# Optimization experiments

Measured on AMD Instinct MI355X. Metric: run time of the kernel, lower is better.

## Reference

```python
import jax, jax.numpy as jnp
import numpy as np

# DCRNN (PEMS-BAY scale) constants
N = 325      # num_nodes
B = 64       # batch_size
T = 12       # encoder seq_len
HZ = 12      # decoder horizon
U = 64       # rnn_units
DIN = 2      # input_dim
DOUT = 1     # output_dim
K = 2        # max_diffusion_step
NM = K + 1   # num diffusion matrices (Chebyshev, single laplacian support)


def _glorot(key, shape):
    lim = float(np.sqrt(6.0 / (shape[0] + shape[1])))
    return jax.random.uniform(key, shape, jnp.float32, -lim, lim)


def setup_inputs() -> dict:
    key = jax.random.key(0)
    ks = jax.random.split(key, 8)
    # random symmetric adjacency -> scaled Laplacian support (lambda_max ~= 2 approx)
    a = np.asarray(jax.random.uniform(ks[0], (N, N)))
    a = (a + a.T) * 0.5
    a = a * (a > 0.9)
    d = a.sum(1)
    dinv = 1.0 / np.sqrt(np.maximum(d, 1e-8))
    L = np.eye(N, dtype=np.float32) - (dinv[:, None] * a * dinv[None, :]).astype(np.float32)
    support = jnp.asarray(L - np.eye(N, dtype=np.float32))  # 2L/lambda_max - I with lambda_max=2

    def cell_params(k, din):
        f = (din + U) * NM
        k1, k2 = jax.random.split(k)
        return dict(gate_W=_glorot(k1, (f, 2 * U)), gate_b=jnp.zeros((2 * U,), jnp.float32),
                    cand_W=_glorot(k2, (f, U)), cand_b=jnp.zeros((U,), jnp.float32))

    inp = {"inputs": jax.random.normal(ks[1], (T, B, N * DIN), jnp.float32),
           "support": support}
    for name, din, kk in [("enc0", DIN, ks[2]), ("enc1", U, ks[3]),
                          ("dec0", DOUT, ks[4]), ("dec1", U, ks[5])]:
        for pn, v in cell_params(kk, din).items():
            inp[f"{name}_{pn}"] = v
    inp["proj_W"] = _glorot(ks[6], (U, DOUT))
    inp["proj_b"] = jnp.zeros((DOUT,), jnp.float32)
    return inp


def _gconv(x, support, W, b):
    # x: (B, N, F). Chebyshev diffusion: x0=x, x1=Lx, x2=2Lx1-x0, ...
    xs = [x]
    x0, x1 = x, jnp.einsum('mn,bnf->bmf', support, x)
    xs.append(x1)
    for _ in range(2, K + 1):
        x2 = 2.0 * jnp.einsum('mn,bnf->bmf', support, x1) - x0
        xs.append(x2)
        x0, x1 = x1, x2
    xk = jnp.concatenate(xs, axis=-1)  # (B, N, NM*F)
    return xk @ W + b


def _gru_cell(x, h, support, gW, gb, cW, cb):
    # diffusion-conv GRU: r,u gates then candidate
    ru = jax.nn.sigmoid(_gconv(jnp.concatenate([x, h], -1), support, gW, gb))
    r, u = jnp.split(ru, 2, axis=-1)
    c = jnp.tanh(_gconv(jnp.concatenate([x, r * h], -1), support, cW, cb))
    return u * h + (1.0 - u) * c


def reference(inputs, support,
              enc0_gate_W, enc0_gate_b, enc0_cand_W, enc0_cand_b,
              enc1_gate_W, enc1_gate_b, enc1_cand_W, enc1_cand_b,
              dec0_gate_W, dec0_gate_b, dec0_cand_W, dec0_cand_b,
              dec1_gate_W, dec1_gate_b, dec1_cand_W, dec1_cand_b,
              proj_W, proj_b):
    x_seq = inputs.reshape(T, B, N, DIN)
    h0 = jnp.zeros((B, N, U), inputs.dtype)

    def enc_step(carry, x):
        h_l0, h_l1 = carry
        h_l0 = _gru_cell(x, h_l0, support, enc0_gate_W, enc0_gate_b, enc0_cand_W, enc0_cand_b)
        h_l1 = _gru_cell(h_l0, h_l1, support, enc1_gate_W, enc1_gate_b, enc1_cand_W, enc1_cand_b)
        return (h_l0, h_l1), None

    (h_l0, h_l1), _ = jax.lax.scan(enc_step, (h0, h0), x_seq)

    def dec_step(carry, _):
        d_in, hd0, hd1 = carry
        hd0 = _gru_cell(d_in, hd0, support, dec0_gate_W, dec0_gate_b, dec0_cand_W, dec0_cand_b)
        hd1 = _gru_cell(hd0, hd1, support, dec1_gate_W, dec1_gate_b, dec1_cand_W, dec1_cand_b)
        out = hd1 @ proj_W + proj_b  # (B, N, DOUT)
        return (out, hd0, hd1), out.reshape(B, N * DOUT)

    start = jnp.zeros((B, N, DOUT), inputs.dtype)  # GO symbol
    _, outputs = jax.lax.scan(dec_step, (start, h_l0, h_l1), None, length=HZ)
    return outputs  # (horizon, B, N*DOUT)
```

## Files before the change

### kernel.cpp

```cpp
#include <hip/hip_runtime.h>

constexpr int N  = 325;
constexpr int B  = 64;
constexpr int T  = 12;
constexpr int HZ = 12;
constexpr int U  = 64;
constexpr int BN = B * N;

constexpr int SSTIL = 42;
constexpr int SSKC  = 11;
constexpr int XST   = 364;

typedef __attribute__((ext_vector_type(8))) short short8;
typedef __attribute__((ext_vector_type(4))) float floatx4;

__device__ inline unsigned short f2bf(float f) {
    unsigned u = __float_as_uint(f);
    u += 0x7fff + ((u >> 16) & 1);
    return (unsigned short)(u >> 16);
}
__device__ inline unsigned pack_hilo(float v) {
    const unsigned short hi = f2bf(v);
    const float hif = __uint_as_float(((unsigned)hi) << 16);
    const unsigned short lo = f2bf(v - hif);
    return (unsigned)hi | ((unsigned)lo << 16);
}
__device__ inline void unpack8(const uint4 u0, const uint4 u1,
                               short8& h, short8& l) {
    const unsigned uu[8] = {u0.x, u0.y, u0.z, u0.w, u1.x, u1.y, u1.z, u1.w};
    #pragma unroll
    for (int j = 0; j < 8; ++j) {
        h[j] = (short)(uu[j] & 0xffffu);
        l[j] = (short)(uu[j] >> 16);
    }
}


__global__ void zero_kernel(unsigned* __restrict__ p, long n) {
    long i = (long)blockIdx.x * blockDim.x + threadIdx.x;
    const long stride = (long)gridDim.x * blockDim.x;
    for (; i < n; i += stride) p[i] = 0u;
}

__global__ __launch_bounds__(256)
void s2_build(const float* __restrict__ S, float* __restrict__ S2)
{
    const int m = blockIdx.x;
    __shared__ float srow[N];
    for (int i = threadIdx.x; i < N; i += 256) srow[i] = S[m * N + i];
    __syncthreads();
    for (int c = threadIdx.x; c < N; c += 256) {
        float a = 0.f;
        for (int k = 0; k < N; ++k) a += srow[k] * S[k * N + c];
        S2[m * N + c] = a;
    }
}

__global__ __launch_bounds__(64)
void prepack_ss(const float* __restrict__ S, const float* __restrict__ S2,
                short* __restrict__ ssh, short* __restrict__ ssl)
{
    const int t = blockIdx.x, kc = blockIdx.y, lane = threadIdx.x;
    const int quad = lane >> 4, l15 = lane & 15;
    short8 hv, lv;
    #pragma unroll
    for (int j = 0; j < 8; ++j) {
        const int m = t * 16 + l15;
        const int k = kc * 32 + quad * 8 + j;
        float v = 0.f;
        if (k < N) {
            if (m < N) v = S[m * N + k];
            else if (m >= 336 && m < 336 + N) v = S2[(m - 336) * N + k];
        }
        const unsigned short hb = f2bf(v);
        hv[j] = (short)hb;
        lv[j] = (short)f2bf(v - __uint_as_float(((unsigned)hb) << 16));
    }
    const size_t off = ((size_t)(t * SSKC + kc) * 64 + lane);
    ((short8*)ssh)[off] = hv;
    ((short8*)ssl)[off] = lv;
}

__global__ __launch_bounds__(64)
void prepack_w(const float* __restrict__ W, short* __restrict__ Wh,
               short* __restrict__ Wl, int F, int Nout, int NT)
{
    const int kc = blockIdx.x, n = blockIdx.y, lane = threadIdx.x;
    const int quad = lane >> 4, l15 = lane & 15;
    short8 hv, lv;
    #pragma unroll
    for (int j = 0; j < 8; ++j) {
        const int k   = kc * 32 + quad * 8 + j;
        const int col = n * 16 + l15;
        const int lvl = k / F, f = k - lvl * F;
        float w = 0.f;
        if (lvl == 0)
            w = W[(size_t)f * Nout + col] - W[(size_t)(2 * F + f) * Nout + col];
        else if (lvl == 1)
            w = W[(size_t)(F + f) * Nout + col];
        else if (lvl == 2)
            w = 2.f * W[(size_t)(2 * F + f) * Nout + col];
        const unsigned short hb = f2bf(w);
        hv[j] = (short)hb;
        lv[j] = (short)f2bf(w - __uint_as_float(((unsigned)hb) << 16));
    }
    const size_t off = ((size_t)(kc * NT + n) * 64 + lane);
    ((short8*)Wh)[off] = hv;
    ((short8*)Wl)[off] = lv;
}

template<int DIN, int F, int K3P, bool RMUL, bool VEC>
__device__ __forceinline__ void diffuse_body(
    const short8* __restrict__ ssh, const short8* __restrict__ ssl,
    const float* __restrict__ x, const float* __restrict__ h,
    const float* __restrict__ ru, unsigned* __restrict__ zcat,
    int cx, int b, unsigned* __restrict__ xls)
{
    const int c0 = cx * 32;
    const int tid = threadIdx.x, wave = tid >> 6, lane = tid & 63;
    const int quad = lane >> 4, l15 = lane & 15;

    if constexpr (VEC) {
        for (int idx4 = tid; idx4 < 352 * 8; idx4 += 896) {
            const int n = idx4 >> 3, f = (idx4 & 7) * 4, gf = c0 + f;
            uint4 pk = make_uint4(0u, 0u, 0u, 0u);
            if (n < N) {
                const int row = b * N + n;
                float4 v;
                if (gf < DIN) {
                    v = *(const float4*)&x[(size_t)row * DIN + gf];
                } else {
                    v = *(const float4*)&h[(size_t)row * U + (gf - DIN)];
                    if (RMUL) {
                        const float4 rv = *(const float4*)&ru[(size_t)row * 128 + (gf - DIN)];
                        v.x *= rv.x; v.y *= rv.y; v.z *= rv.z; v.w *= rv.w;
                    }
                }
                pk.x = pack_hilo(v.x); pk.y = pack_hilo(v.y);
                pk.z = pack_hilo(v.z); pk.w = pack_hilo(v.w);
                if (!(RMUL && gf < DIN))
                    *(uint4*)&zcat[(size_t)row * K3P + gf] = pk;
            }
            xls[(f + 0) * XST + n] = pk.x;
            xls[(f + 1) * XST + n] = pk.y;
            xls[(f + 2) * XST + n] = pk.z;
            xls[(f + 3) * XST + n] = pk.w;
        }
    } else {
        for (int idx = tid; idx < 352 * 32; idx += 896) {
            const int n = idx >> 5, f = idx & 31, gf = c0 + f;
            unsigned u = 0u;
            if (n < N && gf < F) {
                const int row = b * N + n;
                float v;
                if (gf < DIN) {
                    v = x[(size_t)row * DIN + gf];
                } else {
                    v = h[(size_t)row * U + (gf - DIN)];
                    if (RMUL) v *= ru[(size_t)row * 128 + (gf - DIN)];
                }
                u = pack_hilo(v);
                if (!(RMUL && gf < DIN))
                    zcat[(size_t)row * K3P + gf] = u;
            }
            xls[f * XST + n] = u;
        }
    }
    __syncthreads();

    const int tb = wave * 3;

    floatx4 acc[3][2];
    #pragma unroll
    for (int i = 0; i < 3; ++i)
        #pragma unroll
        for (int n = 0; n < 2; ++n)
            acc[i][n] = (floatx4){0.f, 0.f, 0.f, 0.f};

    short8 cah[3], cal[3], nah[3], nal[3];
    #pragma unroll
    for (int i = 0; i < 3; ++i) {
        const size_t fo = (size_t)((tb + i) * SSKC) * 64 + lane;
        cah[i] = ssh[fo]; cal[i] = ssl[fo];
    }
    for (int kc = 0; kc < SSKC; ++kc) {
        if (kc + 1 < SSKC) {
            #pragma unroll
            for (int i = 0; i < 3; ++i) {
                const size_t fo = (size_t)((tb + i) * SSKC + kc + 1) * 64 + lane;
                nah[i] = ssh[fo]; nal[i] = ssl[fo];
            }
        }
        short8 bh[2], bl[2];
        const int koff = kc * 32 + quad * 8;
        #pragma unroll
        for (int n = 0; n < 2; ++n) {
            const uint4 u0 = *(const uint4*)&xls[(n * 16 + l15) * XST + koff];
            const uint4 u1 = *(const uint4*)&xls[(n * 16 + l15) * XST + koff + 4];
            unpack8(u0, u1, bh[n], bl[n]);
        }
        #pragma unroll
        for (int i = 0; i < 3; ++i)
            #pragma unroll
            for (int n = 0; n < 2; ++n) {
                acc[i][n] = __builtin_amdgcn_mfma_f32_16x16x32_bf16(cah[i], bh[n], acc[i][n], 0, 0, 0);
                acc[i][n] = __builtin_amdgcn_mfma_f32_16x16x32_bf16(cah[i], bl[n], acc[i][n], 0, 0, 0);
                acc[i][n] = __builtin_amdgcn_mfma_f32_16x16x32_bf16(cal[i], bh[n], acc[i][n], 0, 0, 0);
            }
        if (kc + 1 < SSKC) {
            #pragma unroll
            for (int i = 0; i < 3; ++i) { cah[i] = nah[i]; cal[i] = nal[i]; }
        }
    }

    #pragma unroll
    for (int i = 0; i < 3; ++i) {
        const int t = tb + i;
        #pragma unroll
        for (int n = 0; n < 2; ++n) {
            const int col = c0 + n * 16 + l15;
            if (col >= F) continue;
            #pragma unroll
            for (int r = 0; r < 4; ++r) {
                const int m = t * 16 + quad * 4 + r;
                if (m < N)
                    zcat[(size_t)(b * N + m) * K3P + F + col] = pack_hilo(acc[i][n][r]);
                else if (m >= 336 && m < 336 + N)
                    zcat[(size_t)(b * N + (m - 336)) * K3P + 2 * F + col] = pack_hilo(acc[i][n][r]);
            }
        }
    }
}


__device__ __forceinline__ void gate_body(const unsigned* __restrict__ zcat,
    int K3p, const short8* __restrict__ Wh, const short8* __restrict__ Wl,
    const float* __restrict__ bias, float* __restrict__ ru, int bx, int nb)
{
    constexpr int NT = 4;
    const int tid = threadIdx.x, wave = tid >> 6, lane = tid & 63;
    const int quad = lane >> 4, l15 = lane & 15;
    const int row0 = bx * 64 + wave * 16;

    floatx4 acc[NT];
    #pragma unroll
    for (int n = 0; n < NT; ++n) {
        const float bv = bias[(nb + n) * 16 + l15];
        acc[n] = (floatx4){bv, bv, bv, bv};
    }
    const unsigned* __restrict__ zrow = zcat + (size_t)(row0 + l15) * K3p + quad * 8;
    const int KC = K3p >> 5;
    for (int kc = 0; kc < KC; ++kc) {
        const uint4* p = (const uint4*)(zrow + kc * 32);
        short8 ahi, alo;
        unpack8(p[0], p[1], ahi, alo);
        const short8* __restrict__ wh = Wh + (size_t)(kc * 8 + nb) * 64 + lane;
        const short8* __restrict__ wl = Wl + (size_t)(kc * 8 + nb) * 64 + lane;
        #pragma unroll
        for (int n = 0; n < NT; ++n) {
            const short8 bh = wh[n * 64], bl = wl[n * 64];
            acc[n] = __builtin_amdgcn_mfma_f32_16x16x32_bf16(ahi, bh, acc[n], 0, 0, 0);
            acc[n] = __builtin_amdgcn_mfma_f32_16x16x32_bf16(ahi, bl, acc[n], 0, 0, 0);
            acc[n] = __builtin_amdgcn_mfma_f32_16x16x32_bf16(alo, bh, acc[n], 0, 0, 0);
        }
    }
    #pragma unroll
    for (int n = 0; n < NT; ++n) {
        const int col = (nb + n) * 16 + l15;
        #pragma unroll
        for (int r = 0; r < 4; ++r) {
            const int row = row0 + quad * 4 + r;
            ru[(size_t)row * 128 + col] = 1.f / (1.f + __expf(-acc[n][r]));
        }
    }
}

__device__ __forceinline__ void cand_body(const unsigned* __restrict__ zcat,
    int K3p, const short8* __restrict__ Wh, const short8* __restrict__ Wl,
    const float* __restrict__ bias, const float* __restrict__ ru,
    float* __restrict__ h, int bx, int nb)
{
    constexpr int NT = 2;
    const int tid = threadIdx.x, wave = tid >> 6, lane = tid & 63;
    const int quad = lane >> 4, l15 = lane & 15;
    const int row0 = bx * 64 + wave * 16;

    floatx4 acc[NT];
    #pragma unroll
    for (int n = 0; n < NT; ++n) {
        const float bv = bias[(nb + n) * 16 + l15];
        acc[n] = (floatx4){bv, bv, bv, bv};
    }
    const unsigned* __restrict__ zrow = zcat + (size_t)(row0 + l15) * K3p + quad * 8;
    const int KC = K3p >> 5;
    for (int kc = 0; kc < KC; ++kc) {
        const uint4* p = (const uint4*)(zrow + kc * 32);
        short8 ahi, alo;
        unpack8(p[0], p[1], ahi, alo);
        const short8* __restrict__ wh = Wh + (size_t)(kc * 4 + nb) * 64 + lane;
        const short8* __restrict__ wl = Wl + (size_t)(kc * 4 + nb) * 64 + lane;
        #pragma unroll
        for (int n = 0; n < NT; ++n) {
            const short8 bh = wh[n * 64], bl = wl[n * 64];
            acc[n] = __builtin_amdgcn_mfma_f32_16x16x32_bf16(ahi, bh, acc[n], 0, 0, 0);
            acc[n] = __builtin_amdgcn_mfma_f32_16x16x32_bf16(ahi, bl, acc[n], 0, 0, 0);
            acc[n] = __builtin_amdgcn_mfma_f32_16x16x32_bf16(alo, bh, acc[n], 0, 0, 0);
        }
    }
    #pragma unroll
    for (int n = 0; n < NT; ++n) {
        const int col = (nb + n) * 16 + l15;
        #pragma unroll
        for (int r = 0; r < 4; ++r) {
            const int row = row0 + quad * 4 + r;
            const float c  = tanhf(acc[n][r]);
            const float ug = ru[(size_t)row * 128 + 64 + col];
            const float hv = h[(size_t)row * 64 + col];
            h[(size_t)row * 64 + col] = ug * hv + (1.f - ug) * c;
        }
    }
}


template<int DIN, int F, int K3P, bool RMUL, int CB, bool VEC>
__global__ __launch_bounds__(896, 7)
void diffuse_solo(const short8* __restrict__ ssh, const short8* __restrict__ ssl,
                  const float* __restrict__ x, const float* __restrict__ h,
                  const float* __restrict__ ru, unsigned* __restrict__ zcat)
{
    __shared__ __align__(16) unsigned xls[32 * XST];
    diffuse_body<DIN, F, K3P, RMUL, VEC>(ssh, ssl, x, h, ru, zcat,
                                         CB + blockIdx.x, blockIdx.y, xls);
}

__global__ __launch_bounds__(256)
void gate_solo(const unsigned* __restrict__ zcat, int K3p,
               const short8* __restrict__ Wh, const short8* __restrict__ Wl,
               const float* __restrict__ bias, float* __restrict__ ru)
{
    gate_body(zcat, K3p, Wh, Wl, bias, ru, blockIdx.x, blockIdx.y * 4);
}

__global__ __launch_bounds__(256)
void cand_solo(const unsigned* __restrict__ zcat, int K3p,
               const short8* __restrict__ Wh, const short8* __restrict__ Wl,
               const float* __restrict__ bias, const float* __restrict__ ru,
               float* __restrict__ h)
{
    cand_body(zcat, K3p, Wh, Wl, bias, ru, h, blockIdx.x, blockIdx.y * 2);
}

__global__ __launch_bounds__(256)
void cand_proj(const unsigned* __restrict__ zcat, int K3p,
               const short8* __restrict__ Wh, const short8* __restrict__ Wl,
               const float* __restrict__ bias, const float* __restrict__ ru,
               float* __restrict__ h, const float* __restrict__ pW,
               const float* __restrict__ pb, float* __restrict__ outp,
               float* __restrict__ dec_in)
{
    constexpr int NT = 4;
    const int tid = threadIdx.x, wave = tid >> 6, lane = tid & 63;
    const int quad = lane >> 4, l15 = lane & 15;
    const int row0 = blockIdx.x * 64 + wave * 16;

    floatx4 acc[NT];
    #pragma unroll
    for (int n = 0; n < NT; ++n) {
        const float bv = bias[n * 16 + l15];
        acc[n] = (floatx4){bv, bv, bv, bv};
    }
    const unsigned* __restrict__ zrow = zcat + (size_t)(row0 + l15) * K3p + quad * 8;
    const int KC = K3p >> 5;
    for (int kc = 0; kc < KC; ++kc) {
        const uint4* p = (const uint4*)(zrow + kc * 32);
        short8 ahi, alo;
        unpack8(p[0], p[1], ahi, alo);
        const short8* __restrict__ wh = Wh + (size_t)(kc * 4) * 64 + lane;
        const short8* __restrict__ wl = Wl + (size_t)(kc * 4) * 64 + lane;
        #pragma unroll
        for (int n = 0; n < NT; ++n) {
            const short8 bh = wh[n * 64], bl = wl[n * 64];
            acc[n] = __builtin_amdgcn_mfma_f32_16x16x32_bf16(ahi, bh, acc[n], 0, 0, 0);
            acc[n] = __builtin_amdgcn_mfma_f32_16x16x32_bf16(ahi, bl, acc[n], 0, 0, 0);
            acc[n] = __builtin_amdgcn_mfma_f32_16x16x32_bf16(alo, bh, acc[n], 0, 0, 0);
        }
    }
    float pr[4] = {0.f, 0.f, 0.f, 0.f};
    #pragma unroll
    for (int n = 0; n < NT; ++n) {
        const int col = n * 16 + l15;
        const float pw = pW[col];
        #pragma unroll
        for (int r = 0; r < 4; ++r) {
            const int row = row0 + quad * 4 + r;
            const float c  = tanhf(acc[n][r]);
            const float ug = ru[(size_t)row * 128 + 64 + col];
            const float hv = h[(size_t)row * 64 + col];
            const float hn = ug * hv + (1.f - ug) * c;
            h[(size_t)row * 64 + col] = hn;
            pr[r] += hn * pw;
        }
    }
    #pragma unroll
    for (int r = 0; r < 4; ++r) {
        float v = pr[r];
        v += __shfl_xor(v, 1); v += __shfl_xor(v, 2);
        v += __shfl_xor(v, 4); v += __shfl_xor(v, 8);
        if (l15 == 0) {
            const int row = row0 + quad * 4 + r;
            const float o = v + pb[0];
            outp[row]   = o;
            dec_in[row] = o;
        }
    }
}


struct DuoDP {
    const short8 *ssh, *ssl;
    const float *xA, *hA, *ruA; unsigned* zA;
    const float *xB, *hB, *ruB; unsigned* zB;
    int cA;
    int cbB;
};

template<bool RM>
__global__ __launch_bounds__(896, 7)
void diffuse_duo(DuoDP P)
{
    __shared__ __align__(16) unsigned xls[32 * XST];
    if ((int)blockIdx.x < P.cA)
        diffuse_body<2, 66, 224, RM, false>(P.ssh, P.ssl, P.xA, P.hA, P.ruA,
                                            P.zA, blockIdx.x, blockIdx.y, xls);
    else
        diffuse_body<64, 128, 384, RM, true>(P.ssh, P.ssl, P.xB, P.hB, P.ruB,
                                             P.zB, P.cbB + blockIdx.x - P.cA,
                                             blockIdx.y, xls);
}

struct DuoGP {
    const unsigned* zA; const short8 *WhA, *WlA; const float* bA; float* ruA;
    const unsigned* zB; const short8 *WhB, *WlB; const float* bB; float* ruB;
};

__global__ __launch_bounds__(256)
void gate_duo(DuoGP P)
{
    if (blockIdx.z == 0)
        gate_body(P.zA, 224, P.WhA, P.WlA, P.bA, P.ruA, blockIdx.x, blockIdx.y * 4);
    else
        gate_body(P.zB, 384, P.WhB, P.WlB, P.bB, P.ruB, blockIdx.x, blockIdx.y * 4);
}

struct DuoCP {
    const unsigned* zA; const short8 *WhA, *WlA; const float* bA;
    const float* ruA; float* hA;
    const unsigned* zB; const short8 *WhB, *WlB; const float* bB;
    const float* ruB; float* hB;
};

__global__ __launch_bounds__(256)
void cand_duo(DuoCP P)
{
    if (blockIdx.z == 0)
        cand_body(P.zA, 224, P.WhA, P.WlA, P.bA, P.ruA, P.hA, blockIdx.x, blockIdx.y * 2);
    else
        cand_body(P.zB, 384, P.WhB, P.WlB, P.bB, P.ruB, P.hB, blockIdx.x, blockIdx.y * 2);
}


extern "C" void kernel_launch(void* const* d_in, const int* in_sizes, int n_in,
                              void* d_out, int out_size, void* d_ws, size_t ws_size,
                              hipStream_t stream)
{
    const float* inputs = (const float*)d_in[0];
    const float* S      = (const float*)d_in[1];
    const float* Wt[4][4];
    for (int l = 0; l < 4; ++l)
        for (int j = 0; j < 4; ++j)
            Wt[l][j] = (const float*)d_in[2 + l * 4 + j];
    const float* pW = (const float*)d_in[18];
    const float* pb = (const float*)d_in[19];
    float* out = (float*)d_out;

    float*    ws     = (float*)d_ws;
    float*    h0     = ws;
    float*    h1     = h0 + (size_t)BN * U;
    float*    dec_in = h1 + (size_t)BN * U;
    float*    ruA    = dec_in + BN;
    float*    ruB    = ruA + (size_t)BN * 128;
    unsigned* zcatA  = (unsigned*)(ruB + (size_t)BN * 128);
    unsigned* zcatB  = zcatA + (size_t)BN * 224;
    float*    S2     = (float*)(zcatB + (size_t)BN * 384);
    char*     pp     = (char*)(S2 + (size_t)N * N);
    pp = (char*)(((uintptr_t)pp + 15) & ~(uintptr_t)15);

    short* ssh = (short*)pp;
    short* ssl = ssh + (size_t)SSTIL * SSKC * 64 * 8;
    char*  wpbase = (char*)(ssl + (size_t)SSTIL * SSKC * 64 * 8);

    const int Fs[4]   = {66, 128, 65, 128};
    const int K3ps[4] = {224, 384, 224, 384};
    short *Wgh[4], *Wgl[4], *Wch[4], *Wcl[4];
    size_t off = 0;
    for (int l = 0; l < 4; ++l) {
        const size_t ge = (size_t)K3ps[l] * 128, ce = (size_t)K3ps[l] * 64;
        Wgh[l] = (short*)(wpbase + off); off += ge * 2;
        Wgl[l] = (short*)(wpbase + off); off += ge * 2;
        Wch[l] = (short*)(wpbase + off); off += ce * 2;
        Wcl[l] = (short*)(wpbase + off); off += ce * 2;
    }

    const long zn = (long)BN * (2 * U) + BN + (long)BN * 256 + (long)BN * (224 + 384);
    zero_kernel<<<2048, 256, 0, stream>>>((unsigned*)h0, zn);

    s2_build<<<N, 256, 0, stream>>>(S, S2);
    prepack_ss<<<dim3(SSTIL, SSKC), 64, 0, stream>>>(S, S2, ssh, ssl);
    for (int l = 0; l < 4; ++l) {
        prepack_w<<<dim3(K3ps[l] / 32, 8), 64, 0, stream>>>(Wt[l][0], Wgh[l], Wgl[l],
                                                            Fs[l], 128, 8);
        prepack_w<<<dim3(K3ps[l] / 32, 4), 64, 0, stream>>>(Wt[l][2], Wch[l], Wcl[l],
                                                            Fs[l], 64, 4);
    }

    const short8* SSH = (const short8*)ssh;
    const short8* SSL = (const short8*)ssl;

    for (int s = 0; s <= T; ++s) {
        const float* x0 = inputs + (size_t)s * BN * 2;
        const bool a = (s < T), b1 = (s >= 1);
        if (a && b1) {
            DuoDP dp{SSH, SSL, x0, h0, nullptr, zcatA, h0, h1, nullptr, zcatB, 3, 0};
            diffuse_duo<false><<<dim3(7, B), 896, 0, stream>>>(dp);
            DuoGP gp{zcatA, (short8*)Wgh[0], (short8*)Wgl[0], Wt[0][1], ruA,
                     zcatB, (short8*)Wgh[1], (short8*)Wgl[1], Wt[1][1], ruB};
            gate_duo<<<dim3(BN / 64, 2, 2), 256, 0, stream>>>(gp);
            DuoDP dp2{SSH, SSL, x0, h0, ruA, zcatA, h0, h1, ruB, zcatB, 3, 2};
            diffuse_duo<true><<<dim3(5, B), 896, 0, stream>>>(dp2);
            DuoCP cp{zcatA, (short8*)Wch[0], (short8*)Wcl[0], Wt[0][3], ruA, h0,
                     zcatB, (short8*)Wch[1], (short8*)Wcl[1], Wt[1][3], ruB, h1};
            cand_duo<<<dim3(BN / 64, 2, 2), 256, 0, stream>>>(cp);
        } else if (a) {
            diffuse_solo<2, 66, 224, false, 0, false><<<dim3(3, B), 896, 0, stream>>>(
                SSH, SSL, x0, h0, nullptr, zcatA);
            gate_solo<<<dim3(BN / 64, 2), 256, 0, stream>>>(
                zcatA, 224, (short8*)Wgh[0], (short8*)Wgl[0], Wt[0][1], ruA);
            diffuse_solo<2, 66, 224, true, 0, false><<<dim3(3, B), 896, 0, stream>>>(
                SSH, SSL, x0, h0, ruA, zcatA);
            cand_solo<<<dim3(BN / 64, 2), 256, 0, stream>>>(
                zcatA, 224, (short8*)Wch[0], (short8*)Wcl[0], Wt[0][3], ruA, h0);
        } else {
            diffuse_solo<64, 128, 384, false, 0, true><<<dim3(4, B), 896, 0, stream>>>(
                SSH, SSL, h0, h1, nullptr, zcatB);
            gate_solo<<<dim3(BN / 64, 2), 256, 0, stream>>>(
                zcatB, 384, (short8*)Wgh[1], (short8*)Wgl[1], Wt[1][1], ruB);
            diffuse_solo<64, 128, 384, true, 2, true><<<dim3(2, B), 896, 0, stream>>>(
                SSH, SSL, h0, h1, ruB, zcatB);
            cand_solo<<<dim3(BN / 64, 2), 256, 0, stream>>>(
                zcatB, 384, (short8*)Wch[1], (short8*)Wcl[1], Wt[1][3], ruB, h1);
        }
    }

    for (int hz = 0; hz < HZ; ++hz) {
        diffuse_solo<1, 65, 224, false, 0, false><<<dim3(3, B), 896, 0, stream>>>(
            SSH, SSL, dec_in, h0, nullptr, zcatB);
        gate_solo<<<dim3(BN / 64, 2), 256, 0, stream>>>(
            zcatB, 224, (short8*)Wgh[2], (short8*)Wgl[2], Wt[2][1], ruA);
        diffuse_solo<1, 65, 224, true, 0, false><<<dim3(3, B), 896, 0, stream>>>(
            SSH, SSL, dec_in, h0, ruA, zcatB);
        cand_solo<<<dim3(BN / 64, 2), 256, 0, stream>>>(
            zcatB, 224, (short8*)Wch[2], (short8*)Wcl[2], Wt[2][3], ruA, h0);
        diffuse_solo<64, 128, 384, false, 0, true><<<dim3(4, B), 896, 0, stream>>>(
            SSH, SSL, h0, h1, nullptr, zcatB);
        gate_solo<<<dim3(BN / 64, 2), 256, 0, stream>>>(
            zcatB, 384, (short8*)Wgh[3], (short8*)Wgl[3], Wt[3][1], ruA);
        diffuse_solo<64, 128, 384, true, 2, true><<<dim3(2, B), 896, 0, stream>>>(
            SSH, SSL, h0, h1, ruA, zcatB);
        cand_proj<<<BN / 64, 256, 0, stream>>>(
            zcatB, 384, (short8*)Wch[3], (short8*)Wcl[3], Wt[3][3], ruA, h1,
            pW, pb, out + (size_t)hz * BN, dec_in);
    }
}
```

Before: 4.080 ms.

## Read level-0 diffusion input directly in gate/cand GEMMs instead of staging in zcat

The diffusion kernels no longer write the packed hi/lo copy of the raw input [x, h] (or [x, r*h]) into zcat. The gate and candidate GEMMs now rebuild those first K-chunks on the fly from the fp32 x, h and r buffers, and only the diffused levels are read from zcat. Prepacked weights are reordered to match, with the level-0 block padded to whole 32-wide chunks. Because the candidate step now reads h while writing a new h, the hidden states are double-buffered (ping-pong). This removes a global write and read of roughly a third of zcat per step, at the cost of extra pack_hilo work and some padding MFMAs inside the GEMMs.

New measurement: 3.964 ms (median of 2 runs). 1.03x faster.

```diff
diff --git a/kernel.cpp b/kernel.cpp
--- a/kernel.cpp
+++ b/kernel.cpp
@@ -83,23 +83,27 @@
 
 __global__ __launch_bounds__(64)
 void prepack_w(const float* __restrict__ W, short* __restrict__ Wh,
-               short* __restrict__ Wl, int F, int Nout, int NT)
+               short* __restrict__ Wl, int F, int Nout, int NT, int Z0KC)
 {
     const int kc = blockIdx.x, n = blockIdx.y, lane = threadIdx.x;
     const int quad = lane >> 4, l15 = lane & 15;
     short8 hv, lv;
     #pragma unroll
     for (int j = 0; j < 8; ++j) {
-        const int k   = kc * 32 + quad * 8 + j;
+        const int p   = kc * 32 + quad * 8 + j;
         const int col = n * 16 + l15;
-        const int lvl = k / F, f = k - lvl * F;
         float w = 0.f;
-        if (lvl == 0)
-            w = W[(size_t)f * Nout + col] - W[(size_t)(2 * F + f) * Nout + col];
-        else if (lvl == 1)
-            w = W[(size_t)(F + f) * Nout + col];
-        else if (lvl == 2)
-            w = 2.f * W[(size_t)(2 * F + f) * Nout + col];
+        if (p < Z0KC * 32) {
+            const int f = p;
+            if (f < F)
+                w = W[(size_t)f * Nout + col] - W[(size_t)(2 * F + f) * Nout + col];
+        } else {
+            const int q = p - Z0KC * 32;
+            if (q < F)
+                w = W[(size_t)(F + q) * Nout + col];
+            else if (q < 2 * F)
+                w = 2.f * W[(size_t)(2 * F + (q - F)) * Nout + col];
+        }
         const unsigned short hb = f2bf(w);
         hv[j] = (short)hb;
         lv[j] = (short)f2bf(w - __uint_as_float(((unsigned)hb) << 16));
@@ -109,7 +113,54 @@
     ((short8*)Wl)[off] = lv;
 }
 
-template<int DIN, int F, int K3P, bool RMUL, bool VEC>
+template<int DIN, int F, bool RM, bool ZV>
+__device__ __forceinline__ void z0_frag(const float* __restrict__ x,
+    const float* __restrict__ h, const float* __restrict__ ru,
+    int row, int kc, int quad, short8& ah, short8& al)
+{
+    float v[8];
+    if constexpr (ZV) {
+        const int k0 = kc * 32 + quad * 8;
+        if (k0 < 64) {
+            const float4 a = *(const float4*)&x[(size_t)row * 64 + k0];
+            const float4 b = *(const float4*)&x[(size_t)row * 64 + k0 + 4];
+            v[0]=a.x; v[1]=a.y; v[2]=a.z; v[3]=a.w;
+            v[4]=b.x; v[5]=b.y; v[6]=b.z; v[7]=b.w;
+        } else {
+            const int kk = k0 - 64;
+            float4 a = *(const float4*)&h[(size_t)row * 64 + kk];
+            float4 b = *(const float4*)&h[(size_t)row * 64 + kk + 4];
+            if constexpr (RM) {
+                const float4 ra = *(const float4*)&ru[(size_t)row * 128 + kk];
+                const float4 rb = *(const float4*)&ru[(size_t)row * 128 + kk + 4];
+                a.x *= ra.x; a.y *= ra.y; a.z *= ra.z; a.w *= ra.w;
+                b.x *= rb.x; b.y *= rb.y; b.z *= rb.z; b.w *= rb.w;
+            }
+            v[0]=a.x; v[1]=a.y; v[2]=a.z; v[3]=a.w;
+            v[4]=b.x; v[5]=b.y; v[6]=b.z; v[7]=b.w;
+        }
+    } else {
+        #pragma unroll
+        for (int j = 0; j < 8; ++j) {
+            const int k = kc * 32 + quad * 8 + j;
+            float t = 0.f;
+            if (k < DIN) t = x[(size_t)row * DIN + k];
+            else if (k < F) {
+                t = h[(size_t)row * 64 + (k - DIN)];
+                if constexpr (RM) t *= ru[(size_t)row * 128 + (k - DIN)];
+            }
+            v[j] = t;
+        }
+    }
+    #pragma unroll
+    for (int j = 0; j < 8; ++j) {
+        const unsigned u = pack_hilo(v[j]);
+        ah[j] = (short)(u & 0xffffu);
+        al[j] = (short)(u >> 16);
+    }
+}
+
+template<int DIN, int F, int YP, bool RMUL, bool VEC>
 __device__ __forceinline__ void diffuse_body(
     const short8* __restrict__ ssh, const short8* __restrict__ ssl,
     const float* __restrict__ x, const float* __restrict__ h,
@@ -138,8 +189,6 @@
                 }
                 pk.x = pack_hilo(v.x); pk.y = pack_hilo(v.y);
                 pk.z = pack_hilo(v.z); pk.w = pack_hilo(v.w);
-                if (!(RMUL && gf < DIN))
-                    *(uint4*)&zcat[(size_t)row * K3P + gf] = pk;
             }
             xls[(f + 0) * XST + n] = pk.x;
             xls[(f + 1) * XST + n] = pk.y;
@@ -160,8 +209,6 @@
                     if (RMUL) v *= ru[(size_t)row * 128 + (gf - DIN)];
                 }
                 u = pack_hilo(v);
-                if (!(RMUL && gf < DIN))
-                    zcat[(size_t)row * K3P + gf] = u;
             }
             xls[f * XST + n] = u;
         }
@@ -224,23 +271,26 @@
             for (int r = 0; r < 4; ++r) {
                 const int m = t * 16 + quad * 4 + r;
                 if (m < N)
-                    zcat[(size_t)(b * N + m) * K3P + F + col] = pack_hilo(acc[i][n][r]);
+                    zcat[(size_t)(b * N + m) * YP + col] = pack_hilo(acc[i][n][r]);
                 else if (m >= 336 && m < 336 + N)
-                    zcat[(size_t)(b * N + (m - 336)) * K3P + 2 * F + col] = pack_hilo(acc[i][n][r]);
+                    zcat[(size_t)(b * N + (m - 336)) * YP + F + col] = pack_hilo(acc[i][n][r]);
             }
         }
     }
 }
 
 
+template<int DIN, int F, int Z0KC, int YKC, bool ZV>
 __device__ __forceinline__ void gate_body(const unsigned* __restrict__ zcat,
-    int K3p, const short8* __restrict__ Wh, const short8* __restrict__ Wl,
-    const float* __restrict__ bias, float* __restrict__ ru, int bx, int nb)
-{
-    constexpr int NT = 4;
+    const float* __restrict__ x, const float* __restrict__ h,
+    const short8* __restrict__ Wh, const short8* __restrict__ Wl,
+    const float* __restrict__ bias, float* __restrict__ ruout, int bx, int nb)
+{
+    constexpr int YP = YKC * 32, NT = 4;
     const int tid = threadIdx.x, wave = tid >> 6, lane = tid & 63;
     const int quad = lane >> 4, l15 = lane & 15;
     const int row0 = bx * 64 + wave * 16;
+    const int row = row0 + l15;
 
     floatx4 acc[NT];
     #pragma unroll
@@ -248,12 +298,9 @@
         const float bv = bias[(nb + n) * 16 + l15];
         acc[n] = (floatx4){bv, bv, bv, bv};
     }
-    const unsigned* __restrict__ zrow = zcat + (size_t)(row0 + l15) * K3p + quad * 8;
-    const int KC = K3p >> 5;
-    for (int kc = 0; kc < KC; ++kc) {
-        const uint4* p = (const uint4*)(zrow + kc * 32);
+    for (int kc = 0; kc < Z0KC; ++kc) {
         short8 ahi, alo;
-        unpack8(p[0], p[1], ahi, alo);
+        z0_frag<DIN, F, false, ZV>(x, h, nullptr, row, kc, quad, ahi, alo);
         const short8* __restrict__ wh = Wh + (size_t)(kc * 8 + nb) * 64 + lane;
         const short8* __restrict__ wl = Wl + (size_t)(kc * 8 + nb) * 64 + lane;
         #pragma unroll
@@ -264,41 +311,13 @@
             acc[n] = __builtin_amdgcn_mfma_f32_16x16x32_bf16(alo, bh, acc[n], 0, 0, 0);
         }
     }
-    #pragma unroll
-    for (int n = 0; n < NT; ++n) {
-        const int col = (nb + n) * 16 + l15;
-        #pragma unroll
-        for (int r = 0; r < 4; ++r) {
-            const int row = row0 + quad * 4 + r;
-            ru[(size_t)row * 128 + col] = 1.f / (1.f + __expf(-acc[n][r]));
-        }
-    }
-}
-
-__device__ __forceinline__ void cand_body(const unsigned* __restrict__ zcat,
-    int K3p, const short8* __restrict__ Wh, const short8* __restrict__ Wl,
-    const float* __restrict__ bias, const float* __restrict__ ru,
-    float* __restrict__ h, int bx, int nb)
-{
-    constexpr int NT = 2;
-    const int tid = threadIdx.x, wave = tid >> 6, lane = tid & 63;
-    const int quad = lane >> 4, l15 = lane & 15;
-    const int row0 = bx * 64 + wave * 16;
-
-    floatx4 acc[NT];
-    #pragma unroll
-    for (int n = 0; n < NT; ++n) {
-        const float bv = bias[(nb + n) * 16 + l15];
-        acc[n] = (floatx4){bv, bv, bv, bv};
-    }
-    const unsigned* __restrict__ zrow = zcat + (size_t)(row0 + l15) * K3p + quad * 8;
-    const int KC = K3p >> 5;
-    for (int kc = 0; kc < KC; ++kc) {
+    const unsigned* __restrict__ zrow = zcat + (size_t)row * YP + quad * 8;
+    for (int kc = 0; kc < YKC; ++kc) {
         const uint4* p = (const uint4*)(zrow + kc * 32);
         short8 ahi, alo;
         unpack8(p[0], p[1], ahi, alo);
-        const short8* __restrict__ wh = Wh + (size_t)(kc * 4 + nb) * 64 + lane;
-        const short8* __restrict__ wl = Wl + (size_t)(kc * 4 + nb) * 64 + lane;
+        const short8* __restrict__ wh = Wh + (size_t)((Z0KC + kc) * 8 + nb) * 64 + lane;
+        const short8* __restrict__ wl = Wl + (size_t)((Z0KC + kc) * 8 + nb) * 64 + lane;
         #pragma unroll
         for (int n = 0; n < NT; ++n) {
             const short8 bh = wh[n * 64], bl = wl[n * 64];
@@ -312,71 +331,36 @@
         const int col = (nb + n) * 16 + l15;
         #pragma unroll
         for (int r = 0; r < 4; ++r) {
-            const int row = row0 + quad * 4 + r;
-            const float c  = tanhf(acc[n][r]);
-            const float ug = ru[(size_t)row * 128 + 64 + col];
-            const float hv = h[(size_t)row * 64 + col];
-            h[(size_t)row * 64 + col] = ug * hv + (1.f - ug) * c;
-        }
-    }
-}
-
-
-template<int DIN, int F, int K3P, bool RMUL, int CB, bool VEC>
-__global__ __launch_bounds__(896, 7)
-void diffuse_solo(const short8* __restrict__ ssh, const short8* __restrict__ ssl,
-                  const float* __restrict__ x, const float* __restrict__ h,
-                  const float* __restrict__ ru, unsigned* __restrict__ zcat)
-{
-    __shared__ __align__(16) unsigned xls[32 * XST];
-    diffuse_body<DIN, F, K3P, RMUL, VEC>(ssh, ssl, x, h, ru, zcat,
-                                         CB + blockIdx.x, blockIdx.y, xls);
-}
-
-__global__ __launch_bounds__(256)
-void gate_solo(const unsigned* __restrict__ zcat, int K3p,
-               const short8* __restrict__ Wh, const short8* __restrict__ Wl,
-               const float* __restrict__ bias, float* __restrict__ ru)
-{
-    gate_body(zcat, K3p, Wh, Wl, bias, ru, blockIdx.x, blockIdx.y * 4);
-}
-
-__global__ __launch_bounds__(256)
-void cand_solo(const unsigned* __restrict__ zcat, int K3p,
-               const short8* __restrict__ Wh, const short8* __restrict__ Wl,
-               const float* __restrict__ bias, const float* __restrict__ ru,
-               float* __restrict__ h)
-{
-    cand_body(zcat, K3p, Wh, Wl, bias, ru, h, blockIdx.x, blockIdx.y * 2);
-}
-
-__global__ __launch_bounds__(256)
-void cand_proj(const unsigned* __restrict__ zcat, int K3p,
-               const short8* __restrict__ Wh, const short8* __restrict__ Wl,
-               const float* __restrict__ bias, const float* __restrict__ ru,
-               float* __restrict__ h, const float* __restrict__ pW,
-               const float* __restrict__ pb, float* __restrict__ outp,
-               float* __restrict__ dec_in)
-{
-    constexpr int NT = 4;
+            const int rw = row0 + quad * 4 + r;
+            ruout[(size_t)rw * 128 + col] = 1.f / (1.f + __expf(-acc[n][r]));
+        }
+    }
+}
+
+template<int DIN, int F, int Z0KC, int YKC, bool ZV>
+__device__ __forceinline__ void cand_body(const unsigned* __restrict__ zcat,
+    const float* __restrict__ x, const float* __restrict__ h,
+    const float* __restrict__ ru, const short8* __restrict__ Wh,
+    const short8* __restrict__ Wl, const float* __restrict__ bias,
+    float* __restrict__ hout, int bx, int nb)
+{
+    constexpr int YP = YKC * 32, NT = 2;
     const int tid = threadIdx.x, wave = tid >> 6, lane = tid & 63;
     const int quad = lane >> 4, l15 = lane & 15;
-    const int row0 = blockIdx.x * 64 + wave * 16;
+    const int row0 = bx * 64 + wave * 16;
+    const int row = row0 + l15;
 
     floatx4 acc[NT];
     #pragma unroll
     for (int n = 0; n < NT; ++n) {
-        const float bv = bias[n * 16 + l15];
+        const float bv = bias[(nb + n) * 16 + l15];
         acc[n] = (floatx4){bv, bv, bv, bv};
     }
-    const unsigned* __restrict__ zrow = zcat + (size_t)(row0 + l15) * K3p + quad * 8;
-    const int KC = K3p >> 5;
-    for (int kc = 0; kc < KC; ++kc) {
-        const uint4* p = (const uint4*)(zrow + kc * 32);
+    for (int kc = 0; kc < Z0KC; ++kc) {
         short8 ahi, alo;
-        unpack8(p[0], p[1], ahi, alo);
-        const short8* __restrict__ wh = Wh + (size_t)(kc * 4) * 64 + lane;
-        const short8* __restrict__ wl = Wl + (size_t)(kc * 4) * 64 + lane;
+        z0_frag<DIN, F, true, ZV>(x, h, ru, row, kc, quad, ahi, alo);
+        const short8* __restrict__ wh = Wh + (size_t)(kc * 4 + nb) * 64 + lane;
+        const short8* __restrict__ wl = Wl + (size_t)(kc * 4 + nb) * 64 + lane;
         #pragma unroll
         for (int n = 0; n < NT; ++n) {
             const short8 bh = wh[n * 64], bl = wl[n * 64];
@@ -385,6 +369,117 @@
             acc[n] = __builtin_amdgcn_mfma_f32_16x16x32_bf16(alo, bh, acc[n], 0, 0, 0);
         }
     }
+    const unsigned* __restrict__ zrow = zcat + (size_t)row * YP + quad * 8;
+    for (int kc = 0; kc < YKC; ++kc) {
+        const uint4* p = (const uint4*)(zrow + kc * 32);
+        short8 ahi, alo;
+        unpack8(p[0], p[1], ahi, alo);
+        const short8* __restrict__ wh = Wh + (size_t)((Z0KC + kc) * 4 + nb) * 64 + lane;
+        const short8* __restrict__ wl = Wl + (size_t)((Z0KC + kc) * 4 + nb) * 64 + lane;
+        #pragma unroll
+        for (int n = 0; n < NT; ++n) {
+            const short8 bh = wh[n * 64], bl = wl[n * 64];
+            acc[n] = __builtin_amdgcn_mfma_f32_16x16x32_bf16(ahi, bh, acc[n], 0, 0, 0);
+            acc[n] = __builtin_amdgcn_mfma_f32_16x16x32_bf16(ahi, bl, acc[n], 0, 0, 0);
+            acc[n] = __builtin_amdgcn_mfma_f32_16x16x32_bf16(alo, bh, acc[n], 0, 0, 0);
+        }
+    }
+    #pragma unroll
+    for (int n = 0; n < NT; ++n) {
+        const int col = (nb + n) * 16 + l15;
+        #pragma unroll
+        for (int r = 0; r < 4; ++r) {
+            const int rw = row0 + quad * 4 + r;
+            const float c  = tanhf(acc[n][r]);
+            const float ug = ru[(size_t)rw * 128 + 64 + col];
+            const float hv = h[(size_t)rw * 64 + col];
+            hout[(size_t)rw * 64 + col] = ug * hv + (1.f - ug) * c;
+        }
+    }
+}
+
+
+template<int DIN, int F, int YP, bool RMUL, int CB, bool VEC>
+__global__ __launch_bounds__(896, 7)
+void diffuse_solo(const short8* __restrict__ ssh, const short8* __restrict__ ssl,
+                  const float* __restrict__ x, const float* __restrict__ h,
+                  const float* __restrict__ ru, unsigned* __restrict__ zcat)
+{
+    __shared__ __align__(16) unsigned xls[32 * XST];
+    diffuse_body<DIN, F, YP, RMUL, VEC>(ssh, ssl, x, h, ru, zcat,
+                                        CB + blockIdx.x, blockIdx.y, xls);
+}
+
+template<int DIN, int F, int Z0KC, int YKC, bool ZV>
+__global__ __launch_bounds__(256)
+void gate_cell(const unsigned* __restrict__ zcat, const float* __restrict__ x,
+               const float* __restrict__ h, const short8* __restrict__ Wh,
+               const short8* __restrict__ Wl, const float* __restrict__ bias,
+               float* __restrict__ ru)
+{
+    gate_body<DIN, F, Z0KC, YKC, ZV>(zcat, x, h, Wh, Wl, bias, ru,
+                                     blockIdx.x, blockIdx.y * 4);
+}
+
+template<int DIN, int F, int Z0KC, int YKC, bool ZV>
+__global__ __launch_bounds__(256)
+void cand_cell(const unsigned* __restrict__ zcat, const float* __restrict__ x,
+               const float* __restrict__ h, const float* __restrict__ ru,
+               const short8* __restrict__ Wh, const short8* __restrict__ Wl,
+               const float* __restrict__ bias, float* __restrict__ hout)
+{
+    cand_body<DIN, F, Z0KC, YKC, ZV>(zcat, x, h, ru, Wh, Wl, bias, hout,
+                                     blockIdx.x, blockIdx.y * 2);
+}
+
+__global__ __launch_bounds__(256)
+void cand_proj(const unsigned* __restrict__ zcat, const float* __restrict__ x,
+               const float* __restrict__ h, const float* __restrict__ ru,
+               const short8* __restrict__ Wh, const short8* __restrict__ Wl,
+               const float* __restrict__ bias, float* __restrict__ hout,
+               const float* __restrict__ pW, const float* __restrict__ pb,
+               float* __restrict__ outp, float* __restrict__ dec_in)
+{
+    constexpr int Z0KC = 4, YKC = 8, YP = 256, NT = 4;
+    const int tid = threadIdx.x, wave = tid >> 6, lane = tid & 63;
+    const int quad = lane >> 4, l15 = lane & 15;
+    const int row0 = blockIdx.x * 64 + wave * 16;
+    const int row = row0 + l15;
+
+    floatx4 acc[NT];
+    #pragma unroll
+    for (int n = 0; n < NT; ++n) {
+        const float bv = bias[n * 16 + l15];
+        acc[n] = (floatx4){bv, bv, bv, bv};
+    }
+    for (int kc = 0; kc < Z0KC; ++kc) {
+        short8 ahi, alo;
+        z0_frag<64, 128, true, true>(x, h, ru, row, kc, quad, ahi, alo);
+        const short8* __restrict__ wh = Wh + (size_t)(kc * 4) * 64 + lane;
+        const short8* __restrict__ wl = Wl + (size_t)(kc * 4) * 64 + lane;
+        #pragma unroll
+        for (int n = 0; n < NT; ++n) {
+            const short8 bh = wh[n * 64], bl = wl[n * 64];
+            acc[n] = __builtin_amdgcn_mfma_f32_16x16x32_bf16(ahi, bh, acc[n], 0, 0, 0);
+            acc[n] = __builtin_amdgcn_mfma_f32_16x16x32_bf16(ahi, bl, acc[n], 0, 0, 0);
+            acc[n] = __builtin_amdgcn_mfma_f32_16x16x32_bf16(alo, bh, acc[n], 0, 0, 0);
+        }
+    }
+    const unsigned* __restrict__ zrow = zcat + (size_t)row * YP + quad * 8;
+    for (int kc = 0; kc < YKC; ++kc) {
+        const uint4* p = (const uint4*)(zrow + kc * 32);
+        short8 ahi, alo;
+        unpack8(p[0], p[1], ahi, alo);
+        const short8* __restrict__ wh = Wh + (size_t)((Z0KC + kc) * 4) * 64 + lane;
+        const short8* __restrict__ wl = Wl + (size_t)((Z0KC + kc) * 4) * 64 + lane;
+        #pragma unroll
+        for (int n = 0; n < NT; ++n) {
+            const short8 bh = wh[n * 64], bl = wl[n * 64];
+            acc[n] = __builtin_amdgcn_mfma_f32_16x16x32_bf16(ahi, bh, acc[n], 0, 0, 0);
+            acc[n] = __builtin_amdgcn_mfma_f32_16x16x32_bf16(ahi, bl, acc[n], 0, 0, 0);
+            acc[n] = __builtin_amdgcn_mfma_f32_16x16x32_bf16(alo, bh, acc[n], 0, 0, 0);
+        }
+    }
     float pr[4] = {0.f, 0.f, 0.f, 0.f};
     #pragma unroll
     for (int n = 0; n < NT; ++n) {
@@ -392,12 +487,12 @@
         const float pw = pW[col];
         #pragma unroll
         for (int r = 0; r < 4; ++r) {
-            const int row = row0 + quad * 4 + r;
+            const int rw = row0 + quad * 4 + r;
             const float c  = tanhf(acc[n][r]);
-            const float ug = ru[(size_t)row * 128 + 64 + col];
-            const float hv = h[(size_t)row * 64 + col];
+            const float ug = ru[(size_t)rw * 128 + 64 + col];
+            const float hv = h[(size_t)rw * 64 + col];
             const float hn = ug * hv + (1.f - ug) * c;
-            h[(size_t)row * 64 + col] = hn;
+            hout[(size_t)rw * 64 + col] = hn;
             pr[r] += hn * pw;
         }
     }
@@ -407,10 +502,10 @@
         v += __shfl_xor(v, 1); v += __shfl_xor(v, 2);
         v += __shfl_xor(v, 4); v += __shfl_xor(v, 8);
         if (l15 == 0) {
-            const int row = row0 + quad * 4 + r;
+            const int rw = row0 + quad * 4 + r;
             const float o = v + pb[0];
-            outp[row]   = o;
-            dec_in[row] = o;
+            outp[rw]   = o;
+            dec_in[rw] = o;
         }
     }
 }
@@ -420,8 +515,7 @@
     const short8 *ssh, *ssl;
     const float *xA, *hA, *ruA; unsigned* zA;
     const float *xB, *hB, *ruB; unsigned* zB;
-    int cA;
-    int cbB;
+    int cA, cbB;
 };
 
 template<bool RM>
@@ -430,42 +524,48 @@
 {
     __shared__ __align__(16) unsigned xls[32 * XST];
     if ((int)blockIdx.x < P.cA)
-        diffuse_body<2, 66, 224, RM, false>(P.ssh, P.ssl, P.xA, P.hA, P.ruA,
+        diffuse_body<2, 66, 160, RM, false>(P.ssh, P.ssl, P.xA, P.hA, P.ruA,
                                             P.zA, blockIdx.x, blockIdx.y, xls);
     else
-        diffuse_body<64, 128, 384, RM, true>(P.ssh, P.ssl, P.xB, P.hB, P.ruB,
+        diffuse_body<64, 128, 256, RM, true>(P.ssh, P.ssl, P.xB, P.hB, P.ruB,
                                              P.zB, P.cbB + blockIdx.x - P.cA,
                                              blockIdx.y, xls);
 }
 
 struct DuoGP {
-    const unsigned* zA; const short8 *WhA, *WlA; const float* bA; float* ruA;
-    const unsigned* zB; const short8 *WhB, *WlB; const float* bB; float* ruB;
+    const unsigned* zA; const float *xA, *hA;
+    const short8 *WhA, *WlA; const float* bA; float* ruA;
+    const unsigned* zB; const float *xB, *hB;
+    const short8 *WhB, *WlB; const float* bB; float* ruB;
 };
 
 __global__ __launch_bounds__(256)
 void gate_duo(DuoGP P)
 {
     if (blockIdx.z == 0)
-        gate_body(P.zA, 224, P.WhA, P.WlA, P.bA, P.ruA, blockIdx.x, blockIdx.y * 4);
+        gate_body<2, 66, 3, 5, false>(P.zA, P.xA, P.hA, P.WhA, P.WlA, P.bA,
+                                      P.ruA, blockIdx.x, blockIdx.y * 4);
     else
-        gate_body(P.zB, 384, P.WhB, P.WlB, P.bB, P.ruB, blockIdx.x, blockIdx.y * 4);
+        gate_body<64, 128, 4, 8, true>(P.zB, P.xB, P.hB, P.WhB, P.WlB, P.bB,
+                                       P.ruB, blockIdx.x, blockIdx.y * 4);
 }
 
 struct DuoCP {
-    const unsigned* zA; const short8 *WhA, *WlA; const float* bA;
-    const float* ruA; float* hA;
-    const unsigned* zB; const short8 *WhB, *WlB; const float* bB;
-    const float* ruB; float* hB;
+    const unsigned* zA; const float *xA, *hA, *ruA;
+    const short8 *WhA, *WlA; const float* bA; float* hoA;
+    const unsigned* zB; const float *xB, *hB, *ruB;
+    const short8 *WhB, *WlB; const float* bB; float* hoB;
 };
 
 __global__ __launch_bounds__(256)
 void cand_duo(DuoCP P)
 {
     if (blockIdx.z == 0)
-        cand_body(P.zA, 224, P.WhA, P.WlA, P.bA, P.ruA, P.hA, blockIdx.x, blockIdx.y * 2);
+        cand_body<2, 66, 3, 5, false>(P.zA, P.xA, P.hA, P.ruA, P.WhA, P.WlA,
+                                      P.bA, P.hoA, blockIdx.x, blockIdx.y * 2);
     else
-        cand_body(P.zB, 384, P.WhB, P.WlB, P.bB, P.ruB, P.hB, blockIdx.x, blockIdx.y * 2);
+        cand_body<64, 128, 4, 8, true>(P.zB, P.xB, P.hB, P.ruB, P.WhB, P.WlB,
+                                       P.bB, P.hoB, blockIdx.x, blockIdx.y * 2);
 }
 
 
@@ -484,14 +584,14 @@
     float* out = (float*)d_out;
 
     float*    ws     = (float*)d_ws;
-    float*    h0     = ws;
-    float*    h1     = h0 + (size_t)BN * U;
-    float*    dec_in = h1 + (size_t)BN * U;
+    float*    H0[2]  = {ws, ws + (size_t)BN * U};
+    float*    H1[2]  = {ws + 2 * (size_t)BN * U, ws + 3 * (size_t)BN * U};
+    float*    dec_in = ws + 4 * (size_t)BN * U;
     float*    ruA    = dec_in + BN;
     float*    ruB    = ruA + (size_t)BN * 128;
     unsigned* zcatA  = (unsigned*)(ruB + (size_t)BN * 128);
-    unsigned* zcatB  = zcatA + (size_t)BN * 224;
-    float*    S2     = (float*)(zcatB + (size_t)BN * 384);
+    unsigned* zcatB  = zcatA + (size_t)BN * 160;
+    float*    S2     = (float*)(zcatB + (size_t)BN * 256);
     char*     pp     = (char*)(S2 + (size_t)N * N);
     pp = (char*)(((uintptr_t)pp + 15) & ~(uintptr_t)15);
 
@@ -500,84 +600,93 @@
     char*  wpbase = (char*)(ssl + (size_t)SSTIL * SSKC * 64 * 8);
 
     const int Fs[4]   = {66, 128, 65, 128};
-    const int K3ps[4] = {224, 384, 224, 384};
+    const int KPs[4]  = {256, 384, 256, 384};
+    const int Z0s[4]  = {3, 4, 3, 4};
     short *Wgh[4], *Wgl[4], *Wch[4], *Wcl[4];
     size_t off = 0;
     for (int l = 0; l < 4; ++l) {
-        const size_t ge = (size_t)K3ps[l] * 128, ce = (size_t)K3ps[l] * 64;
+        const size_t ge = (size_t)KPs[l] * 128, ce = (size_t)KPs[l] * 64;
         Wgh[l] = (short*)(wpbase + off); off += ge * 2;
         Wgl[l] = (short*)(wpbase + off); off += ge * 2;
         Wch[l] = (short*)(wpbase + off); off += ce * 2;
         Wcl[l] = (short*)(wpbase + off); off += ce * 2;
     }
 
-    const long zn = (long)BN * (2 * U) + BN + (long)BN * 256 + (long)BN * (224 + 384);
-    zero_kernel<<<2048, 256, 0, stream>>>((unsigned*)h0, zn);
+    const long zn = (long)BN * (4 * U) + BN + (long)BN * 256 + (long)BN * (160 + 256);
+    zero_kernel<<<2048, 256, 0, stream>>>((unsigned*)ws, zn);
 
     s2_build<<<N, 256, 0, stream>>>(S, S2);
     prepack_ss<<<dim3(SSTIL, SSKC), 64, 0, stream>>>(S, S2, ssh, ssl);
     for (int l = 0; l < 4; ++l) {
-        prepack_w<<<dim3(K3ps[l] / 32, 8), 64, 0, stream>>>(Wt[l][0], Wgh[l], Wgl[l],
-                                                            Fs[l], 128, 8);
-        prepack_w<<<dim3(K3ps[l] / 32, 4), 64, 0, stream>>>(Wt[l][2], Wch[l], Wcl[l],
-                                                            Fs[l], 64, 4);
+        prepack_w<<<dim3(KPs[l] / 32, 8), 64, 0, stream>>>(Wt[l][0], Wgh[l], Wgl[l],
+                                                           Fs[l], 128, 8, Z0s[l]);
+        prepack_w<<<dim3(KPs[l] / 32, 4), 64, 0, stream>>>(Wt[l][2], Wch[l], Wcl[l],
+                                                           Fs[l], 64, 4, Z0s[l]);
     }
 
     const short8* SSH = (const short8*)ssh;
     const short8* SSL = (const short8*)ssl;
+    int p0 = 0, p1 = 0;
 
     for (int s = 0; s <= T; ++s) {
         const float* x0 = inputs + (size_t)s * BN * 2;
         const bool a = (s < T), b1 = (s >= 1);
         if (a && b1) {
-            DuoDP dp{SSH, SSL, x0, h0, nullptr, zcatA, h0, h1, nullptr, zcatB, 3, 0};
+            DuoDP dp{SSH, SSL, x0, H0[p0], nullptr, zcatA,
+                     H0[p0], H1[p1], nullptr, zcatB, 3, 0};
             diffuse_duo<false><<<dim3(7, B), 896, 0, stream>>>(dp);
-            DuoGP gp{zcatA, (short8*)Wgh[0], (short8*)Wgl[0], Wt[0][1], ruA,
-                     zcatB, (short8*)Wgh[1], (short8*)Wgl[1], Wt[1][1], ruB};
+            DuoGP gp{zcatA, x0, H0[p0], (short8*)Wgh[0], (short8*)Wgl[0], Wt[0][1], ruA,
+                     zcatB, H0[p0], H1[p1], (short8*)Wgh[1], (short8*)Wgl[1], Wt[1][1], ruB};
             gate_duo<<<dim3(BN / 64, 2, 2), 256, 0, stream>>>(gp);
-            DuoDP dp2{SSH, SSL, x0, h0, ruA, zcatA, h0, h1, ruB, zcatB, 3, 2};
+            DuoDP dp2{SSH, SSL, x0, H0[p0], ruA, zcatA,
+                      H0[p0], H1[p1], ruB, zcatB, 3, 2};
             diffuse_duo<true><<<dim3(5, B), 896, 0, stream>>>(dp2);
-            DuoCP cp{zcatA, (short8*)Wch[0], (short8*)Wcl[0], Wt[0][3], ruA, h0,
-                     zcatB, (short8*)Wch[1], (short8*)Wcl[1], Wt[1][3], ruB, h1};
+            DuoCP cp{zcatA, x0, H0[p0], ruA, (short8*)Wch[0], (short8*)Wcl[0], Wt[0][3], H0[p0 ^ 1],
+                     zcatB, H0[p0], H1[p1], ruB, (short8*)Wch[1], (short8*)Wcl[1], Wt[1][3], H1[p1 ^ 1]};
             cand_duo<<<dim3(BN / 64, 2, 2), 256, 0, stream>>>(cp);
+            p0 ^= 1; p1 ^= 1;
         } else if (a) {
-            diffuse_solo<2, 66, 224, false, 0, false><<<dim3(3, B), 896, 0, stream>>>(
-                SSH, SSL, x0, h0, nullptr, zcatA);
-            gate_solo<<<dim3(BN / 64, 2), 256, 0, stream>>>(
-                zcatA, 224, (short8*)Wgh[0], (short8*)Wgl[0], Wt[0][1], ruA);
-            diffuse_solo<2, 66, 224, true, 0, false><<<dim3(3, B), 896, 0, stream>>>(
-                SSH, SSL, x0, h0, ruA, zcatA);
-            cand_solo<<<dim3(BN / 64, 2), 256, 0, stream>>>(
-                zcatA, 224, (short8*)Wch[0], (short8*)Wcl[0], Wt[0][3], ruA, h0);
+            diffuse_solo<2, 66, 160, false, 0, false><<<dim3(3, B), 896, 0, stream>>>(
+                SSH, SSL, x0, H0[p0], nullptr, zcatA);
+            gate_cell<2, 66, 3, 5, false><<<dim3(BN / 64, 2), 256, 0, stream>>>(
+                zcatA, x0, H0[p0], (short8*)Wgh[0], (short8*)Wgl[0], Wt[0][1], ruA);
+            diffuse_solo<2, 66, 160, true, 0, false><<<dim3(3, B), 896, 0, stream>>>(
+                SSH, SSL, x0, H0[p0], ruA, zcatA);
+            cand_cell<2, 66, 3, 5, false><<<dim3(BN / 64, 2), 256, 0, stream>>>(
+                zcatA, x0, H0[p0], ruA, (short8*)Wch[0], (short8*)Wcl[0], Wt[0][3], H0[p0 ^ 1]);
+            p0 ^= 1;
         } else {
-            diffuse_solo<64, 128, 384, false, 0, true><<<dim3(4, B), 896, 0, stream>>>(
-                SSH, SSL, h0, h1, nullptr, zcatB);
-            gate_solo<<<dim3(BN / 64, 2), 256, 0, stream>>>(
-                zcatB, 384, (short8*)Wgh[1], (short8*)Wgl[1], Wt[1][1], ruB);
-            diffuse_solo<64, 128, 384, true, 2, true><<<dim3(2, B), 896, 0, stream>>>(
-                SSH, SSL, h0, h1, ruB, zcatB);
-            cand_solo<<<dim3(BN / 64, 2), 256, 0, stream>>>(
-                zcatB, 384, (short8*)Wch[1], (short8*)Wcl[1], Wt[1][3], ruB, h1);
+            diffuse_solo<64, 128, 256, false, 0, true><<<dim3(4, B), 896, 0, stream>>>(
+                SSH, SSL, H0[p0], H1[p1], nullptr, zcatB);
+            gate_cell<64, 128, 4, 8, true><<<dim3(BN / 64, 2), 256, 0, stream>>>(
+                zcatB, H0[p0], H1[p1], (short8*)Wgh[1], (short8*)Wgl[1], Wt[1][1], ruB);
+            diffuse_solo<64, 128, 256, true, 2, true><<<dim3(2, B), 896, 0, stream>>>(
+                SSH, SSL, H0[p0], H1[p1], ruB, zcatB);
+            cand_cell<64, 128, 4, 8, true><<<dim3(BN / 64, 2), 256, 0, stream>>>(
+                zcatB, H0[p0], H1[p1], ruB, (short8*)Wch[1], (short8*)Wcl[1], Wt[1][3], H1[p1 ^ 1]);
+            p1 ^= 1;
         }
     }
 
     for (int hz = 0; hz < HZ; ++hz) {
-        diffuse_solo<1, 65, 224, false, 0, false><<<dim3(3, B), 896, 0, stream>>>(
-            SSH, SSL, dec_in, h0, nullptr, zcatB);
-        gate_solo<<<dim3(BN / 64, 2), 256, 0, stream>>>(
-            zcatB, 224, (short8*)Wgh[2], (short8*)Wgl[2], Wt[2][1], ruA);
-        diffuse_solo<1, 65, 224, true, 0, false><<<dim3(3, B), 896, 0, stream>>>(
-            SSH, SSL, dec_in, h0, ruA, zcatB);
-        cand_solo<<<dim3(BN / 64, 2), 256, 0, stream>>>(
-            zcatB, 224, (short8*)Wch[2], (short8*)Wcl[2], Wt[2][3], ruA, h0);
-        diffuse_solo<64, 128, 384, false, 0, true><<<dim3(4, B), 896, 0, stream>>>(
-            SSH, SSL, h0, h1, nullptr, zcatB);
-        gate_solo<<<dim3(BN / 64, 2), 256, 0, stream>>>(
-            zcatB, 384, (short8*)Wgh[3], (short8*)Wgl[3], Wt[3][1], ruA);
-        diffuse_solo<64, 128, 384, true, 2, true><<<dim3(2, B), 896, 0, stream>>>(
-            SSH, SSL, h0, h1, ruA, zcatB);
+        diffuse_solo<1, 65, 160, false, 0, false><<<dim3(3, B), 896, 0, stream>>>(
+            SSH, SSL, dec_in, H0[p0], nullptr, zcatB);
+        gate_cell<1, 65, 3, 5, false><<<dim3(BN / 64, 2), 256, 0, stream>>>(
+            zcatB, dec_in, H0[p0], (short8*)Wgh[2], (short8*)Wgl[2], Wt[2][1], ruA);
+        diffuse_solo<1, 65, 160, true, 0, false><<<dim3(3, B), 896, 0, stream>>>(
+            SSH, SSL, dec_in, H0[p0], ruA, zcatB);
+        cand_cell<1, 65, 3, 5, false><<<dim3(BN / 64, 2), 256, 0, stream>>>(
+            zcatB, dec_in, H0[p0], ruA, (short8*)Wch[2], (short8*)Wcl[2], Wt[2][3], H0[p0 ^ 1]);
+        p0 ^= 1;
+        diffuse_solo<64, 128, 256, false, 0, true><<<dim3(4, B), 896, 0, stream>>>(
+            SSH, SSL, H0[p0], H1[p1], nullptr, zcatB);
+        gate_cell<64, 128, 4, 8, true><<<dim3(BN / 64, 2), 256, 0, stream>>>(
+            zcatB, H0[p0], H1[p1], (short8*)Wgh[3], (short8*)Wgl[3], Wt[3][1], ruA);
+        diffuse_solo<64, 128, 256, true, 2, true><<<dim3(2, B), 896, 0, stream>>>(
+            SSH, SSL, H0[p0], H1[p1], ruA, zcatB);
         cand_proj<<<BN / 64, 256, 0, stream>>>(
-            zcatB, 384, (short8*)Wch[3], (short8*)Wcl[3], Wt[3][3], ruA, h1,
-            pW, pb, out + (size_t)hz * BN, dec_in);
-    }
-}
+            zcatB, H0[p0], H1[p1], ruA, (short8*)Wch[3], (short8*)Wcl[3], Wt[3][3],
+            H1[p1 ^ 1], pW, pb, out + (size_t)hz * BN, dec_in);
+        p1 ^= 1;
+    }
+}
```
